# Kernel optimization log

Measured on AMD Instinct MI355X. Metric: run time of the kernel, lower is better.

The kernel has to match this reference:

```python
import jax, jax.numpy as jnp
import numpy as np

N_NODES = 100000
N_EDGES = 625000
NODE_DIM = 128
N_REL = 16
SLOPE = 0.2


def setup_inputs() -> dict:
    key = jax.random.key(0)
    k1, k2, k3, k4 = jax.random.split(key, 4)
    x_base = jax.random.normal(k1, (N_NODES, NODE_DIM), dtype=jnp.float32)
    # xavier-uniform-like init for a_r_params [n_rel, 2*node_dim]
    limit = float(np.sqrt(6.0 / (N_REL + 2 * NODE_DIM)))
    a_r_params = jax.random.uniform(k2, (N_REL, 2 * NODE_DIM), dtype=jnp.float32,
                                    minval=-limit, maxval=limit)
    rel_edge_index = jax.random.randint(k3, (2, N_EDGES), 0, N_NODES, dtype=jnp.int64 if jax.config.jax_enable_x64 else jnp.int32).astype(jnp.int32)
    rel_edge_type = jax.random.randint(k4, (N_EDGES,), 0, N_REL).astype(jnp.int32)
    return {"x_base": x_base, "a_r_params": a_r_params,
            "rel_edge_index": rel_edge_index, "rel_edge_type": rel_edge_type}


def reference(x_base, a_r_params, rel_edge_index, rel_edge_type):
    n_nodes, d = x_base.shape
    src = rel_edge_index[0]
    dst = rel_edge_index[1]
    # gather per-edge node features and per-edge relation params
    x_u = x_base[src]                       # [E, d]
    x_v = x_base[dst]                       # [E, d]
    a_r = a_r_params[rel_edge_type]         # [E, 2d]
    # sum(a_r * cat([x_u, x_v])) without materializing the concat
    e = jnp.sum(a_r[:, :d] * x_u, axis=-1) + jnp.sum(a_r[:, d:] * x_v, axis=-1)  # [E]
    e_act = jnp.where(e >= 0, e, SLOPE * e)  # leaky relu
    # scatter softmax over src groups (stable: subtract per-segment max)
    seg_max = jax.ops.segment_max(e_act, src, num_segments=n_nodes)  # [N]
    ex = jnp.exp(e_act - seg_max[src])
    seg_sum = jax.ops.segment_sum(ex, src, num_segments=n_nodes)     # [N]
    alpha = ex / seg_sum[src]
    return alpha
```

## Files before the change

### kernel.cpp

```cpp
#include <hip/hip_runtime.h>
#include <hip/hip_fp16.h>

#define NN 100000
#define NE 625000
#define ND 128
#define NR 16
#define SLOPE 0.2f
#define NB 782
#define CAP 1280
#define MAXE 5
#define PRE_BLOCKS 1563
#define SC_EPB 4096
#define SC_BLOCKS 153
#define LSTR 136

using s16x8 = __attribute__((ext_vector_type(8))) short;
using f32x4 = __attribute__((ext_vector_type(4))) float;

__global__ void zero_cursor(unsigned* __restrict__ c) {
    int i = blockIdx.x * 256 + threadIdx.x;
    if (i < NB) c[i] = 0u;
}

__device__ __forceinline__ void bf_split(float x, unsigned short& h, unsigned short& l) {
    unsigned u = __float_as_uint(x);
    h = (unsigned short)(u >> 16);
    float hf = __uint_as_float(u & 0xFFFF0000u);
    l = (unsigned short)(__float_as_uint(x - hf) >> 16);
}

__global__ __launch_bounds__(256) void pre_scatter(
        const float* __restrict__ x, const float* __restrict__ a,
        const int* __restrict__ srcs, const int* __restrict__ dsts,
        const int* __restrict__ etype,
        __half* __restrict__ table, int2* __restrict__ bedge,
        unsigned* __restrict__ cursor) {
    __shared__ __align__(16) unsigned short smem[2 * 32 * LSTR];
    int tid = threadIdx.x;
    int b = blockIdx.x;

    if (b >= SC_BLOCKS) {
        unsigned short* Wh = smem;
        unsigned short* Wl = Wh + 32 * LSTR;
        int nb = (b - SC_BLOCKS) * 64;

#pragma unroll
        for (int i = 0; i < 4; ++i) {
            int f = tid + i * 256;
            int row = f >> 6;
            int c4 = f & 63;
            int o = row + ((c4 >> 5) << 4);
            int k = (c4 & 31) << 2;
            float4 v = *(const float4*)&a[(size_t)row * 256 + (size_t)c4 * 4];
            unsigned short h0, l0, h1, l1, h2, l2, h3, l3;
            bf_split(v.x, h0, l0); bf_split(v.y, h1, l1);
            bf_split(v.z, h2, l2); bf_split(v.w, h3, l3);
            *(uint2*)&Wh[o * LSTR + k] =
                make_uint2((unsigned)h0 | ((unsigned)h1 << 16),
                           (unsigned)h2 | ((unsigned)h3 << 16));
            *(uint2*)&Wl[o * LSTR + k] =
                make_uint2((unsigned)l0 | ((unsigned)l1 << 16),
                           (unsigned)l2 | ((unsigned)l3 << 16));
        }
        __syncthreads();

        int w = tid >> 6;
        int lane = tid & 63;
        int r16 = lane & 15;
        int q = lane >> 4;

        int n = nb + w * 16 + r16;
        bool vld = n < NN;
        const float* xrow = x + (size_t)(vld ? n : 0) * ND + q * 8;

        f32x4 acc0 = {0.f, 0.f, 0.f, 0.f};
        f32x4 acc1 = {0.f, 0.f, 0.f, 0.f};
        const unsigned short* w0h = &Wh[r16 * LSTR + q * 8];
        const unsigned short* w0l = &Wl[r16 * LSTR + q * 8];
        const unsigned short* w1h = &Wh[(16 + r16) * LSTR + q * 8];
        const unsigned short* w1l = &Wl[(16 + r16) * LSTR + q * 8];
#pragma unroll
        for (int ks = 0; ks < 4; ++ks) {
            float4 v0 = vld ? *(const float4*)&xrow[ks * 32]
                            : make_float4(0.f, 0.f, 0.f, 0.f);
            float4 v1 = vld ? *(const float4*)&xrow[ks * 32 + 4]
                            : make_float4(0.f, 0.f, 0.f, 0.f);
            s16x8 ah, al;
            unsigned short h, lo;
            bf_split(v0.x, h, lo); ah[0] = (short)h; al[0] = (short)lo;
            bf_split(v0.y, h, lo); ah[1] = (short)h; al[1] = (short)lo;
            bf_split(v0.z, h, lo); ah[2] = (short)h; al[2] = (short)lo;
            bf_split(v0.w, h, lo); ah[3] = (short)h; al[3] = (short)lo;
            bf_split(v1.x, h, lo); ah[4] = (short)h; al[4] = (short)lo;
            bf_split(v1.y, h, lo); ah[5] = (short)h; al[5] = (short)lo;
            bf_split(v1.z, h, lo); ah[6] = (short)h; al[6] = (short)lo;
            bf_split(v1.w, h, lo); ah[7] = (short)h; al[7] = (short)lo;

            s16x8 bh0 = *(const s16x8*)&w0h[ks * 32];
            s16x8 bl0 = *(const s16x8*)&w0l[ks * 32];
            s16x8 bh1 = *(const s16x8*)&w1h[ks * 32];
            s16x8 bl1 = *(const s16x8*)&w1l[ks * 32];
            acc0 = __builtin_amdgcn_mfma_f32_16x16x32_bf16(ah, bh0, acc0, 0, 0, 0);
            acc0 = __builtin_amdgcn_mfma_f32_16x16x32_bf16(al, bh0, acc0, 0, 0, 0);
            acc0 = __builtin_amdgcn_mfma_f32_16x16x32_bf16(ah, bl0, acc0, 0, 0, 0);
            acc1 = __builtin_amdgcn_mfma_f32_16x16x32_bf16(ah, bh1, acc1, 0, 0, 0);
            acc1 = __builtin_amdgcn_mfma_f32_16x16x32_bf16(al, bh1, acc1, 0, 0, 0);
            acc1 = __builtin_amdgcn_mfma_f32_16x16x32_bf16(ah, bl1, acc1, 0, 0, 0);
        }
        int nrow = nb + w * 16 + q * 4;
#pragma unroll
        for (int r = 0; r < 4; ++r) {
            int nn = nrow + r;
            if (nn < NN) {
                table[(size_t)nn * 32 + r16]      = __float2half_rn(acc0[r]);
                table[(size_t)nn * 32 + 16 + r16] = __float2half_rn(acc1[r]);
            }
        }
    } else {
        unsigned* hist = (unsigned*)smem;
        for (int j = tid; j < NB; j += 256) hist[j] = 0u;
        __syncthreads();

        int base = b * SC_EPB;
#pragma unroll
        for (int i = 0; i < 4; ++i) {
            int e = base + (i * 256 + tid) * 4;
            if (e < NE) {
                int4 s4 = *(const int4*)&srcs[e];
                atomicAdd(&hist[s4.x >> 7], 1u);
                atomicAdd(&hist[s4.y >> 7], 1u);
                atomicAdd(&hist[s4.z >> 7], 1u);
                atomicAdd(&hist[s4.w >> 7], 1u);
            }
        }
        __syncthreads();
        for (int j = tid; j < NB; j += 256) {
            unsigned c = hist[j];
            hist[j] = c ? atomicAdd(&cursor[j], c) : 0u;
        }
        __syncthreads();
#pragma unroll
        for (int i = 0; i < 4; ++i) {
            int e = base + (i * 256 + tid) * 4;
            if (e < NE) {
                int4 s4 = *(const int4*)&srcs[e];
                int4 d4 = *(const int4*)&dsts[e];
                int4 r4 = *(const int4*)&etype[e];
                int ss[4] = {s4.x, s4.y, s4.z, s4.w};
                int dd[4] = {d4.x, d4.y, d4.z, d4.w};
                int rr[4] = {r4.x, r4.y, r4.z, r4.w};
#pragma unroll
                for (int j = 0; j < 4; ++j) {
                    int bk = ss[j] >> 7;
                    unsigned slot = atomicAdd(&hist[bk], 1u);
                    if (slot < CAP) {
                        int w0 = (ss[j] & 127) | (rr[j] << 7) | (dd[j] << 11);
                        bedge[(size_t)bk * CAP + slot] = make_int2(w0, e + j);
                    }
                }
            }
        }
    }
}

__global__ __launch_bounds__(256) void fused_abc(
        const unsigned* __restrict__ cursor, const int2* __restrict__ bedge,
        const __half* __restrict__ table, float* __restrict__ out) {
    __shared__ float lsum[128];
    int b = blockIdx.x;
    int tid = threadIdx.x;
    if (tid < 128) lsum[tid] = 0.f;
    __syncthreads();

    unsigned count = cursor[b];
    if (count > CAP) count = CAP;
    const int2* bin = bedge + (size_t)b * CAP;

    int2 ed[MAXE];
    float u[MAXE], v[MAXE], ex[MAXE];

#pragma unroll
    for (int k = 0; k < MAXE; ++k) {
        unsigned i = tid + 256u * k;
        if (i < count) ed[k] = bin[i];
    }
#pragma unroll
    for (int k = 0; k < MAXE; ++k) {
        unsigned i = tid + 256u * k;
        if (i < count) {
            int w = ed[k].x;
            int sl = w & 127;
            int r  = (w >> 7) & 15;
            int d  = w >> 11;
            u[k] = __half2float(table[(size_t)((b << 7) + sl) * 32 + r]);
            v[k] = __half2float(table[(size_t)d * 32 + 16 + r]);
        }
    }
#pragma unroll
    for (int k = 0; k < MAXE; ++k) {
        unsigned i = tid + 256u * k;
        if (i < count) {
            float av = u[k] + v[k];
            av = (av >= 0.f) ? av : SLOPE * av;
            ex[k] = __expf(av);
            atomicAdd(&lsum[ed[k].x & 127], ex[k]);
        }
    }
    __syncthreads();
#pragma unroll
    for (int k = 0; k < MAXE; ++k) {
        unsigned i = tid + 256u * k;
        if (i < count)
            out[ed[k].y] = __fdividef(ex[k], lsum[ed[k].x & 127]);
    }
}

extern "C" void kernel_launch(void* const* d_in, const int* in_sizes, int n_in,
                              void* d_out, int out_size, void* d_ws, size_t ws_size,
                              hipStream_t stream) {
    const float* x     = (const float*)d_in[0];
    const float* a     = (const float*)d_in[1];
    const int*   eidx  = (const int*)d_in[2];
    const int*   etype = (const int*)d_in[3];
    const int*   srcs  = eidx;
    const int*   dsts  = eidx + NE;
    float*       out   = (float*)d_out;

    char* ws = (char*)d_ws;
    __half*   table  = (__half*)(ws);
    int2*     bedge  = (int2*)(ws + 6400000);
    unsigned* cursor = (unsigned*)(ws + 14407680);

    dim3 blk(256);
    zero_cursor<<<dim3(4), blk, 0, stream>>>(cursor);
    pre_scatter<<<dim3(PRE_BLOCKS + SC_BLOCKS), blk, 0, stream>>>(
        x, a, srcs, dsts, etype, table, bedge, cursor);
    fused_abc<<<dim3(NB), blk, 0, stream>>>(cursor, bedge, table, out);
}
```

Measured before the change: 44.14 us.

## Precompute split relation weights once and double node tile per block

Moves the bf16 hi/lo split of the relation parameters into the cursor-zeroing prep kernel, which writes it once to workspace. The projection blocks then read the split weights directly from global/L2 instead of rebuilding them in shared memory in every block. Each projection block now handles 128 nodes, two 16-row MFMA tiles per wave, so the weight fragments are reused across twice as many nodes and the block count halves. The cost is more registers per thread and global weight loads in place of LDS reads, and the prep kernel's split runs serially in a single block.

```diff
diff --git a/kernel.cpp b/kernel.cpp
--- a/kernel.cpp
+++ b/kernel.cpp
@@ -9,18 +9,12 @@
 #define NB 782
 #define CAP 1280
 #define MAXE 5
-#define PRE_BLOCKS 1563
+#define PRE_BLOCKS 782
 #define SC_EPB 4096
 #define SC_BLOCKS 153
-#define LSTR 136
 
 using s16x8 = __attribute__((ext_vector_type(8))) short;
 using f32x4 = __attribute__((ext_vector_type(4))) float;
-
-__global__ void zero_cursor(unsigned* __restrict__ c) {
-    int i = blockIdx.x * 256 + threadIdx.x;
-    if (i < NB) c[i] = 0u;
-}
 
 __device__ __forceinline__ void bf_split(float x, unsigned short& h, unsigned short& l) {
     unsigned u = __float_as_uint(x);
@@ -29,95 +23,119 @@
     l = (unsigned short)(__float_as_uint(x - hf) >> 16);
 }
 
+__global__ void prep(const float* __restrict__ a, unsigned* __restrict__ cursor,
+                     unsigned short* __restrict__ wsplit) {
+    int t = blockIdx.x * 256 + threadIdx.x;
+    if (t < NB) cursor[t] = 0u;
+    if (blockIdx.x == 0) {
+        for (int i = threadIdx.x; i < 4096; i += 256) {
+            int row = i >> 8, col = i & 255;
+            int o = row + ((col >> 7) << 4);
+            int k = col & 127;
+            unsigned short h, l;
+            bf_split(a[i], h, l);
+            wsplit[o * 128 + k] = h;
+            wsplit[4096 + o * 128 + k] = l;
+        }
+    }
+}
+
 __global__ __launch_bounds__(256) void pre_scatter(
-        const float* __restrict__ x, const float* __restrict__ a,
+        const float* __restrict__ x, const unsigned short* __restrict__ wsplit,
         const int* __restrict__ srcs, const int* __restrict__ dsts,
         const int* __restrict__ etype,
         __half* __restrict__ table, int2* __restrict__ bedge,
         unsigned* __restrict__ cursor) {
-    __shared__ __align__(16) unsigned short smem[2 * 32 * LSTR];
+    __shared__ unsigned hist[NB];
     int tid = threadIdx.x;
     int b = blockIdx.x;
 
     if (b >= SC_BLOCKS) {
-        unsigned short* Wh = smem;
-        unsigned short* Wl = Wh + 32 * LSTR;
-        int nb = (b - SC_BLOCKS) * 64;
-
-#pragma unroll
-        for (int i = 0; i < 4; ++i) {
-            int f = tid + i * 256;
-            int row = f >> 6;
-            int c4 = f & 63;
-            int o = row + ((c4 >> 5) << 4);
-            int k = (c4 & 31) << 2;
-            float4 v = *(const float4*)&a[(size_t)row * 256 + (size_t)c4 * 4];
-            unsigned short h0, l0, h1, l1, h2, l2, h3, l3;
-            bf_split(v.x, h0, l0); bf_split(v.y, h1, l1);
-            bf_split(v.z, h2, l2); bf_split(v.w, h3, l3);
-            *(uint2*)&Wh[o * LSTR + k] =
-                make_uint2((unsigned)h0 | ((unsigned)h1 << 16),
-                           (unsigned)h2 | ((unsigned)h3 << 16));
-            *(uint2*)&Wl[o * LSTR + k] =
-                make_uint2((unsigned)l0 | ((unsigned)l1 << 16),
-                           (unsigned)l2 | ((unsigned)l3 << 16));
-        }
-        __syncthreads();
-
+        int nb = (b - SC_BLOCKS) * 128;
         int w = tid >> 6;
         int lane = tid & 63;
         int r16 = lane & 15;
         int q = lane >> 4;
 
-        int n = nb + w * 16 + r16;
-        bool vld = n < NN;
-        const float* xrow = x + (size_t)(vld ? n : 0) * ND + q * 8;
-
-        f32x4 acc0 = {0.f, 0.f, 0.f, 0.f};
-        f32x4 acc1 = {0.f, 0.f, 0.f, 0.f};
-        const unsigned short* w0h = &Wh[r16 * LSTR + q * 8];
-        const unsigned short* w0l = &Wl[r16 * LSTR + q * 8];
-        const unsigned short* w1h = &Wh[(16 + r16) * LSTR + q * 8];
-        const unsigned short* w1l = &Wl[(16 + r16) * LSTR + q * 8];
+        int n0 = nb + w * 16 + r16;
+        int n1 = n0 + 64;
+        bool v0 = n0 < NN, v1 = n1 < NN;
+        const float* xr0 = x + (size_t)(v0 ? n0 : 0) * ND + q * 8;
+        const float* xr1 = x + (size_t)(v1 ? n1 : 0) * ND + q * 8;
+
+        const unsigned short* Wh = wsplit;
+        const unsigned short* Wl = wsplit + 4096;
+        const unsigned short* w0h = Wh + r16 * 128 + q * 8;
+        const unsigned short* w0l = Wl + r16 * 128 + q * 8;
+        const unsigned short* w1h = Wh + (16 + r16) * 128 + q * 8;
+        const unsigned short* w1l = Wl + (16 + r16) * 128 + q * 8;
+
+        f32x4 acc00 = {0.f,0.f,0.f,0.f};
+        f32x4 acc01 = {0.f,0.f,0.f,0.f};
+        f32x4 acc10 = {0.f,0.f,0.f,0.f};
+        f32x4 acc11 = {0.f,0.f,0.f,0.f};
 #pragma unroll
         for (int ks = 0; ks < 4; ++ks) {
-            float4 v0 = vld ? *(const float4*)&xrow[ks * 32]
-                            : make_float4(0.f, 0.f, 0.f, 0.f);
-            float4 v1 = vld ? *(const float4*)&xrow[ks * 32 + 4]
-                            : make_float4(0.f, 0.f, 0.f, 0.f);
-            s16x8 ah, al;
+            float4 p0 = v0 ? *(const float4*)&xr0[ks * 32]
+                           : make_float4(0.f,0.f,0.f,0.f);
+            float4 p1 = v0 ? *(const float4*)&xr0[ks * 32 + 4]
+                           : make_float4(0.f,0.f,0.f,0.f);
+            float4 p2 = v1 ? *(const float4*)&xr1[ks * 32]
+                           : make_float4(0.f,0.f,0.f,0.f);
+            float4 p3 = v1 ? *(const float4*)&xr1[ks * 32 + 4]
+                           : make_float4(0.f,0.f,0.f,0.f);
+            s16x8 ah0, al0, ah1, al1;
             unsigned short h, lo;
-            bf_split(v0.x, h, lo); ah[0] = (short)h; al[0] = (short)lo;
-            bf_split(v0.y, h, lo); ah[1] = (short)h; al[1] = (short)lo;
-            bf_split(v0.z, h, lo); ah[2] = (short)h; al[2] = (short)lo;
-            bf_split(v0.w, h, lo); ah[3] = (short)h; al[3] = (short)lo;
-            bf_split(v1.x, h, lo); ah[4] = (short)h; al[4] = (short)lo;
-            bf_split(v1.y, h, lo); ah[5] = (short)h; al[5] = (short)lo;
-            bf_split(v1.z, h, lo); ah[6] = (short)h; al[6] = (short)lo;
-            bf_split(v1.w, h, lo); ah[7] = (short)h; al[7] = (short)lo;
+            bf_split(p0.x,h,lo); ah0[0]=(short)h; al0[0]=(short)lo;
+            bf_split(p0.y,h,lo); ah0[1]=(short)h; al0[1]=(short)lo;
+            bf_split(p0.z,h,lo); ah0[2]=(short)h; al0[2]=(short)lo;
+            bf_split(p0.w,h,lo); ah0[3]=(short)h; al0[3]=(short)lo;
+            bf_split(p1.x,h,lo); ah0[4]=(short)h; al0[4]=(short)lo;
+            bf_split(p1.y,h,lo); ah0[5]=(short)h; al0[5]=(short)lo;
+            bf_split(p1.z,h,lo); ah0[6]=(short)h; al0[6]=(short)lo;
+            bf_split(p1.w,h,lo); ah0[7]=(short)h; al0[7]=(short)lo;
+            bf_split(p2.x,h,lo); ah1[0]=(short)h; al1[0]=(short)lo;
+            bf_split(p2.y,h,lo); ah1[1]=(short)h; al1[1]=(short)lo;
+            bf_split(p2.z,h,lo); ah1[2]=(short)h; al1[2]=(short)lo;
+            bf_split(p2.w,h,lo); ah1[3]=(short)h; al1[3]=(short)lo;
+            bf_split(p3.x,h,lo); ah1[4]=(short)h; al1[4]=(short)lo;
+            bf_split(p3.y,h,lo); ah1[5]=(short)h; al1[5]=(short)lo;
+            bf_split(p3.z,h,lo); ah1[6]=(short)h; al1[6]=(short)lo;
+            bf_split(p3.w,h,lo); ah1[7]=(short)h; al1[7]=(short)lo;
 
             s16x8 bh0 = *(const s16x8*)&w0h[ks * 32];
             s16x8 bl0 = *(const s16x8*)&w0l[ks * 32];
             s16x8 bh1 = *(const s16x8*)&w1h[ks * 32];
             s16x8 bl1 = *(const s16x8*)&w1l[ks * 32];
-            acc0 = __builtin_amdgcn_mfma_f32_16x16x32_bf16(ah, bh0, acc0, 0, 0, 0);
-            acc0 = __builtin_amdgcn_mfma_f32_16x16x32_bf16(al, bh0, acc0, 0, 0, 0);
-            acc0 = __builtin_amdgcn_mfma_f32_16x16x32_bf16(ah, bl0, acc0, 0, 0, 0);
-            acc1 = __builtin_amdgcn_mfma_f32_16x16x32_bf16(ah, bh1, acc1, 0, 0, 0);
-            acc1 = __builtin_amdgcn_mfma_f32_16x16x32_bf16(al, bh1, acc1, 0, 0, 0);
-            acc1 = __builtin_amdgcn_mfma_f32_16x16x32_bf16(ah, bl1, acc1, 0, 0, 0);
-        }
-        int nrow = nb + w * 16 + q * 4;
+
+            acc00 = __builtin_amdgcn_mfma_f32_16x16x32_bf16(ah0, bh0, acc00, 0,0,0);
+            acc00 = __builtin_amdgcn_mfma_f32_16x16x32_bf16(al0, bh0, acc00, 0,0,0);
+            acc00 = __builtin_amdgcn_mfma_f32_16x16x32_bf16(ah0, bl0, acc00, 0,0,0);
+            acc01 = __builtin_amdgcn_mfma_f32_16x16x32_bf16(ah0, bh1, acc01, 0,0,0);
+            acc01 = __builtin_amdgcn_mfma_f32_16x16x32_bf16(al0, bh1, acc01, 0,0,0);
+            acc01 = __builtin_amdgcn_mfma_f32_16x16x32_bf16(ah0, bl1, acc01, 0,0,0);
+            acc10 = __builtin_amdgcn_mfma_f32_16x16x32_bf16(ah1, bh0, acc10, 0,0,0);
+            acc10 = __builtin_amdgcn_mfma_f32_16x16x32_bf16(al1, bh0, acc10, 0,0,0);
+            acc10 = __builtin_amdgcn_mfma_f32_16x16x32_bf16(ah1, bl0, acc10, 0,0,0);
+            acc11 = __builtin_amdgcn_mfma_f32_16x16x32_bf16(ah1, bh1, acc11, 0,0,0);
+            acc11 = __builtin_amdgcn_mfma_f32_16x16x32_bf16(al1, bh1, acc11, 0,0,0);
+            acc11 = __builtin_amdgcn_mfma_f32_16x16x32_bf16(ah1, bl1, acc11, 0,0,0);
+        }
+        int nr0 = nb + w * 16 + q * 4;
 #pragma unroll
         for (int r = 0; r < 4; ++r) {
-            int nn = nrow + r;
+            int nn = nr0 + r;
             if (nn < NN) {
-                table[(size_t)nn * 32 + r16]      = __float2half_rn(acc0[r]);
-                table[(size_t)nn * 32 + 16 + r16] = __float2half_rn(acc1[r]);
+                table[(size_t)nn * 32 + r16]      = __float2half_rn(acc00[r]);
+                table[(size_t)nn * 32 + 16 + r16] = __float2half_rn(acc01[r]);
+            }
+            int nn1 = nn + 64;
+            if (nn1 < NN) {
+                table[(size_t)nn1 * 32 + r16]      = __float2half_rn(acc10[r]);
+                table[(size_t)nn1 * 32 + 16 + r16] = __float2half_rn(acc11[r]);
             }
         }
     } else {
-        unsigned* hist = (unsigned*)smem;
         for (int j = tid; j < NB; j += 256) hist[j] = 0u;
         __syncthreads();
 
@@ -227,13 +245,14 @@
     float*       out   = (float*)d_out;
 
     char* ws = (char*)d_ws;
-    __half*   table  = (__half*)(ws);
-    int2*     bedge  = (int2*)(ws + 6400000);
-    unsigned* cursor = (unsigned*)(ws + 14407680);
+    __half*         table  = (__half*)(ws);
+    int2*           bedge  = (int2*)(ws + 6400000);
+    unsigned*       cursor = (unsigned*)(ws + 14407680);
+    unsigned short* wsplit = (unsigned short*)(ws + 14410880);
 
     dim3 blk(256);
-    zero_cursor<<<dim3(4), blk, 0, stream>>>(cursor);
+    prep<<<dim3(4), blk, 0, stream>>>(a, cursor, wsplit);
     pre_scatter<<<dim3(PRE_BLOCKS + SC_BLOCKS), blk, 0, stream>>>(
-        x, a, srcs, dsts, etype, table, bedge, cursor);
+        x, wsplit, srcs, dsts, etype, table, bedge, cursor);
     fused_abc<<<dim3(NB), blk, 0, stream>>>(cursor, bedge, table, out);
 }
```

Measured after the change: 47.05 us. 1.07x slower.
